# Kernel tuning notes

Hardware: AMD Instinct MI355X
Metric: run time of the kernel (lower is better)

## Reference

```python
import jax, jax.numpy as jnp
import numpy as np

C = 256   # hidden_size (in_channels)
V = 97    # VOC_SIZE + 1
T = 32    # encoder time steps
N = 4096  # batch of text instances


def setup_inputs() -> dict:
    key = jax.random.key(0)
    ks = jax.random.split(key, 10)
    s = lambda k, shape: jax.random.normal(k, shape, dtype=jnp.float32) * 0.05
    return {
        "input": jax.random.randint(ks[0], (N,), 0, V),
        "hidden": s(ks[1], (1, N, C)),
        "encoder_outputs": s(ks[2], (T, N, C)),
        "emb": s(ks[3], (V, C)),
        "combine_w": s(ks[4], (C, 2 * C)), "combine_b": jnp.zeros((C,), jnp.float32),
        "vat_w": s(ks[5], (1, C)), "vat_b": jnp.zeros((1,), jnp.float32),
        "gru_w_ih": s(ks[6], (3 * C, C)), "gru_w_hh": s(ks[7], (3 * C, C)),
        "gru_b_ih": jnp.zeros((3 * C,), jnp.float32), "gru_b_hh": jnp.zeros((3 * C,), jnp.float32),
        "out_w": s(ks[8], (V, C)), "out_b": jnp.zeros((V,), jnp.float32),
    }


def reference(input, hidden, encoder_outputs, emb, combine_w, combine_b,
              vat_w, vat_b, gru_w_ih, gru_w_hh, gru_b_ih, gru_b_hh,
              out_w, out_b):
    # Embedding lookup (dropout = identity in eval mode)
    embedded = emb[input]                                   # [N, C]

    # Bahdanau additive attention: vat(tanh(hidden + enc))
    alpha = jnp.tanh(hidden + encoder_outputs)              # [T, N, C]
    scores = jnp.einsum('tnc,c->nt', alpha, vat_w[0]) + vat_b[0]  # [N, T]
    attn = jax.nn.softmax(scores, axis=1)                   # [N, T]
    applied = jnp.einsum('nt,tnc->nc', attn, encoder_outputs)     # [N, C]

    # Combine + relu
    x = jnp.concatenate([embedded, applied], axis=1) @ combine_w.T + combine_b  # [N, C]
    x = jax.nn.relu(x)

    # Single-step GRU cell (PyTorch gate ordering: r, z, n)
    h = hidden[0]                                           # [N, C]
    gi = x @ gru_w_ih.T + gru_b_ih                          # [N, 3C]
    gh = h @ gru_w_hh.T + gru_b_hh                          # [N, 3C]
    ir, iz, i_n = jnp.split(gi, 3, axis=1)
    hr, hz, h_n = jnp.split(gh, 3, axis=1)
    r = jax.nn.sigmoid(ir + hr)
    z = jax.nn.sigmoid(iz + hz)
    n = jnp.tanh(i_n + r * h_n)
    h_new = (1.0 - z) * n + z * h                           # [N, C]

    out = jax.nn.log_softmax(h_new @ out_w.T + out_b, axis=1)  # [N, V]
    return out, h_new[None, :, :], attn[:, None, :]
```

## Files before the change

kernel.cpp:

```cpp
#include <hip/hip_runtime.h>

typedef unsigned short u16;
using bf16x8 = __attribute__((ext_vector_type(8))) __bf16;
using f32x4  = __attribute__((ext_vector_type(4))) float;

__device__ __forceinline__ u16 f2bf(float f) {
  union { float f; unsigned int i; } v; v.f = f;
  unsigned int r = v.i + 0x7fffu + ((v.i >> 16) & 1u);
  return (u16)(r >> 16);
}
__device__ __forceinline__ void cvt8(u16* dst, const float* src) {
  float4 a0 = *reinterpret_cast<const float4*>(src);
  float4 a1 = *reinterpret_cast<const float4*>(src + 4);
  dst[0] = f2bf(a0.x); dst[1] = f2bf(a0.y); dst[2] = f2bf(a0.z); dst[3] = f2bf(a0.w);
  dst[4] = f2bf(a1.x); dst[5] = f2bf(a1.y); dst[6] = f2bf(a1.z); dst[7] = f2bf(a1.w);
}

__global__ __launch_bounds__(256) void k_attn(
    const float* __restrict__ enc, const float* __restrict__ hid,
    const float* __restrict__ vw, const float* __restrict__ vb,
    const float* __restrict__ emb, const int* __restrict__ inp,
    float* __restrict__ attn_out, u16* __restrict__ Acomb)
{
  __shared__ float enc_s[32 * 260];
  __shared__ float part_s[32 * 8];
  __shared__ float sc_s[32];
  __shared__ float at_s[32];
  __shared__ float h_s[256];
  __shared__ float w_s[256];

  const int n = blockIdx.x;
  const int tid = threadIdx.x;

  #pragma unroll
  for (int it = 0; it < 8; ++it) {
    int ci = tid + it * 256;
    int t = ci >> 6, c4 = ci & 63;
    *reinterpret_cast<float4*>(&enc_s[t * 260 + c4 * 4]) =
      *reinterpret_cast<const float4*>(&enc[(t * 4096 + n) * 256 + c4 * 4]);
  }
  h_s[tid] = hid[n * 256 + tid];
  w_s[tid] = vw[tid];
  __syncthreads();

  {
    int t = tid & 31, p = tid >> 5;
    float s = 0.f;
    for (int j = 0; j < 32; ++j) {
      int c = p * 32 + j;
      s += tanhf(h_s[c] + enc_s[t * 260 + c]) * w_s[c];
    }
    part_s[t * 8 + p] = s;
  }
  __syncthreads();

  if (tid < 32) {
    float sc = vb[0];
    for (int j = 0; j < 8; ++j) sc += part_s[tid * 8 + j];
    sc_s[tid] = sc;
  }
  __syncthreads();

  if (tid < 32) {
    float mx = -1e30f;
    for (int j = 0; j < 32; ++j) mx = fmaxf(mx, sc_s[j]);
    float sum = 0.f;
    for (int j = 0; j < 32; ++j) sum += expf(sc_s[j] - mx);
    float a = expf(sc_s[tid] - mx) / sum;
    at_s[tid] = a;
    attn_out[n * 32 + tid] = a;
  }
  __syncthreads();

  float acc = 0.f;
  for (int t = 0; t < 32; ++t) acc += at_s[t] * enc_s[t * 260 + tid];
  Acomb[n * 512 + 256 + tid] = f2bf(acc);
  Acomb[n * 512 + tid] = f2bf(emb[inp[n] * 256 + tid]);
}

__global__ __launch_bounds__(256) void k_combine(
    const u16* __restrict__ A, const float* __restrict__ W,
    const float* __restrict__ bias, u16* __restrict__ X)
{
  __shared__ u16 As[64 * 40];
  __shared__ u16 Bs[64 * 40];

  const int tid = threadIdx.x;
  const int lane = tid & 63;
  const int wave = tid >> 6;
  const int lr = lane & 15, quad = lane >> 4;
  const int m0 = blockIdx.x * 64;
  const int j0 = blockIdx.y * 64;
  const int wm = (wave & 1) * 32;
  const int wn = (wave >> 1) * 32;
  const int sr = tid >> 2, sq = tid & 3;

  for (int i = tid; i < 64 * 40; i += 256) { As[i] = 0; Bs[i] = 0; }
  __syncthreads();

  f32x4 acc[2][2] = {};

  for (int kt = 0; kt < 16; ++kt) {
    int k0 = kt * 32;
    *reinterpret_cast<uint4*>(&As[sr * 40 + sq * 8]) =
      *reinterpret_cast<const uint4*>(&A[(m0 + sr) * 512 + k0 + sq * 8]);
    cvt8(&Bs[sr * 40 + sq * 8], &W[(j0 + sr) * 512 + k0 + sq * 8]);
    __syncthreads();
    bf16x8 aF[2], bF[2];
    #pragma unroll
    for (int s = 0; s < 2; ++s) {
      aF[s] = *reinterpret_cast<const bf16x8*>(&As[(wm + s * 16 + lr) * 40 + quad * 8]);
      bF[s] = *reinterpret_cast<const bf16x8*>(&Bs[(wn + s * 16 + lr) * 40 + quad * 8]);
    }
    #pragma unroll
    for (int sm = 0; sm < 2; ++sm)
      #pragma unroll
      for (int sn = 0; sn < 2; ++sn)
        acc[sm][sn] = __builtin_amdgcn_mfma_f32_16x16x32_bf16(aF[sm], bF[sn], acc[sm][sn], 0, 0, 0);
    __syncthreads();
  }

  #pragma unroll
  for (int sm = 0; sm < 2; ++sm) {
    #pragma unroll
    for (int sn = 0; sn < 2; ++sn) {
      int gc = j0 + wn + sn * 16 + lr;
      float bv = bias[gc];
      int gr = m0 + wm + sm * 16 + quad * 4;
      #pragma unroll
      for (int r = 0; r < 4; ++r) {
        float v = acc[sm][sn][r] + bv;
        X[(gr + r) * 256 + gc] = f2bf(fmaxf(v, 0.f));
      }
    }
  }
}

__global__ __launch_bounds__(256) void k_gru(
    const u16* __restrict__ X, const float* __restrict__ Hin,
    const float* __restrict__ Wih, const float* __restrict__ Whh,
    const float* __restrict__ bih, const float* __restrict__ bhh,
    float* __restrict__ Hout)
{
  __shared__ u16 Xs[64 * 40];
  __shared__ u16 Hs[64 * 40];
  __shared__ u16 Bs[6 * 32 * 40];

  const int tid = threadIdx.x;
  const int lane = tid & 63;
  const int wave = tid >> 6;
  const int lr = lane & 15, quad = lane >> 4;
  const int m0 = blockIdx.x * 64;
  const int c0 = blockIdx.y * 32;

  for (int i = tid; i < 64 * 40; i += 256) { Xs[i] = 0; Hs[i] = 0; }
  for (int i = tid; i < 6 * 32 * 40; i += 256) Bs[i] = 0;
  __syncthreads();

  f32x4 aI[3][2] = {};
  f32x4 aH[3][2] = {};

  for (int kt = 0; kt < 8; ++kt) {
    int k0 = kt * 32;
    for (int ci = tid; ci < 1280; ci += 256) {
      if (ci < 256) {
        int r = ci >> 2, q = ci & 3;
        *reinterpret_cast<uint4*>(&Xs[r * 40 + q * 8]) =
          *reinterpret_cast<const uint4*>(&X[(m0 + r) * 256 + k0 + q * 8]);
      } else if (ci < 512) {
        int b = ci - 256;
        int r = b >> 2, q = b & 3;
        cvt8(&Hs[r * 40 + q * 8], &Hin[(m0 + r) * 256 + k0 + q * 8]);
      } else {
        int b = ci - 512;
        int g = b >> 7, r = (b >> 2) & 31, q = b & 3;
        const float* Wsrc = (g < 3) ? Wih : Whh;
        int gg = (g < 3) ? g : g - 3;
        cvt8(&Bs[(g * 32 + r) * 40 + q * 8],
             &Wsrc[(gg * 256 + c0 + r) * 256 + k0 + q * 8]);
      }
    }
    __syncthreads();
    bf16x8 xF = *reinterpret_cast<const bf16x8*>(&Xs[(wave * 16 + lr) * 40 + quad * 8]);
    bf16x8 hF = *reinterpret_cast<const bf16x8*>(&Hs[(wave * 16 + lr) * 40 + quad * 8]);
    #pragma unroll
    for (int g = 0; g < 3; ++g) {
      #pragma unroll
      for (int sn = 0; sn < 2; ++sn) {
        bf16x8 bI = *reinterpret_cast<const bf16x8*>(&Bs[(g * 32 + sn * 16 + lr) * 40 + quad * 8]);
        bf16x8 bH = *reinterpret_cast<const bf16x8*>(&Bs[((g + 3) * 32 + sn * 16 + lr) * 40 + quad * 8]);
        aI[g][sn] = __builtin_amdgcn_mfma_f32_16x16x32_bf16(xF, bI, aI[g][sn], 0, 0, 0);
        aH[g][sn] = __builtin_amdgcn_mfma_f32_16x16x32_bf16(hF, bH, aH[g][sn], 0, 0, 0);
      }
    }
    __syncthreads();
  }

  #pragma unroll
  for (int sn = 0; sn < 2; ++sn) {
    int gc = c0 + sn * 16 + lr;
    float b_ir = bih[gc],       b_hr = bhh[gc];
    float b_iz = bih[256 + gc], b_hz = bhh[256 + gc];
    float b_in = bih[512 + gc], b_hn = bhh[512 + gc];
    #pragma unroll
    for (int r = 0; r < 4; ++r) {
      int grow = m0 + wave * 16 + quad * 4 + r;
      float rg = 1.f / (1.f + expf(-(aI[0][sn][r] + b_ir + aH[0][sn][r] + b_hr)));
      float zg = 1.f / (1.f + expf(-(aI[1][sn][r] + b_iz + aH[1][sn][r] + b_hz)));
      float ng = tanhf(aI[2][sn][r] + b_in + rg * (aH[2][sn][r] + b_hn));
      float hv = Hin[grow * 256 + gc];
      Hout[grow * 256 + gc] = (1.f - zg) * ng + zg * hv;
    }
  }
}

__global__ __launch_bounds__(256) void k_out(
    const float* __restrict__ H, const float* __restrict__ Wo,
    const float* __restrict__ bo, float* __restrict__ O)
{
  __shared__ u16 As[64 * 40];
  __shared__ u16 Bs[128 * 40];
  __shared__ float L[64 * 101];
  __shared__ float lz_s[64];

  const int tid = threadIdx.x;
  const int lane = tid & 63;
  const int wave = tid >> 6;
  const int lr = lane & 15, quad = lane >> 4;
  const int m0 = blockIdx.x * 64;

  for (int i = tid; i < 64 * 40; i += 256) As[i] = 0;
  for (int i = tid; i < 128 * 40; i += 256) Bs[i] = 0;
  for (int i = tid; i < 64 * 101; i += 256) L[i] = 0.f;
  if (tid < 64) lz_s[tid] = 0.f;
  __syncthreads();

  f32x4 acc[8] = {};

  for (int kt = 0; kt < 8; ++kt) {
    int k0 = kt * 32;
    {
      int r = tid >> 2, q = tid & 3;
      cvt8(&As[r * 40 + q * 8], &H[(m0 + r) * 256 + k0 + q * 8]);
      #pragma unroll
      for (int it = 0; it < 2; ++it) {
        int ci = tid + it * 256;
        int br = ci >> 2, bq = ci & 3;
        if (br < 97) {
          cvt8(&Bs[br * 40 + bq * 8], &Wo[br * 256 + k0 + bq * 8]);
        } else {
          u16* bd = &Bs[br * 40 + bq * 8];
          #pragma unroll
          for (int z = 0; z < 8; ++z) bd[z] = 0;
        }
      }
    }
    __syncthreads();
    bf16x8 aF = *reinterpret_cast<const bf16x8*>(&As[(wave * 16 + lr) * 40 + quad * 8]);
    #pragma unroll
    for (int s = 0; s < 8; ++s) {
      bf16x8 bF = *reinterpret_cast<const bf16x8*>(&Bs[(s * 16 + lr) * 40 + quad * 8]);
      acc[s] = __builtin_amdgcn_mfma_f32_16x16x32_bf16(aF, bF, acc[s], 0, 0, 0);
    }
    __syncthreads();
  }

  #pragma unroll
  for (int s = 0; s < 8; ++s) {
    int col = s * 16 + lr;
    if (col < 97) {
      float bv = bo[col];
      #pragma unroll
      for (int r = 0; r < 4; ++r) {
        int row = wave * 16 + quad * 4 + r;
        L[row * 101 + col] = acc[s][r] + bv;
      }
    }
  }
  __syncthreads();

  if (tid < 64) {
    float mx = -1e30f;
    for (int c = 0; c < 97; ++c) mx = fmaxf(mx, L[tid * 101 + c]);
    float sum = 0.f;
    for (int c = 0; c < 97; ++c) sum += expf(L[tid * 101 + c] - mx);
    lz_s[tid] = mx + logf(sum);
  }
  __syncthreads();

  {
    int row = tid >> 2, sub = tid & 3;
    float lz = lz_s[row];
    int grow = m0 + row;
    for (int c = sub; c < 97; c += 4)
      O[grow * 97 + c] = L[row * 101 + c] - lz;
  }
}

extern "C" void kernel_launch(void* const* d_in, const int* in_sizes, int n_in,
                              void* d_out, int out_size, void* d_ws, size_t ws_size,
                              hipStream_t stream) {
  const int*   inp = (const int*)d_in[0];
  const float* hid = (const float*)d_in[1];
  const float* enc = (const float*)d_in[2];
  const float* emb = (const float*)d_in[3];
  const float* cw  = (const float*)d_in[4];
  const float* cb  = (const float*)d_in[5];
  const float* vw  = (const float*)d_in[6];
  const float* vb  = (const float*)d_in[7];
  const float* wih = (const float*)d_in[8];
  const float* whh = (const float*)d_in[9];
  const float* bih = (const float*)d_in[10];
  const float* bhh = (const float*)d_in[11];
  const float* ow  = (const float*)d_in[12];
  const float* ob  = (const float*)d_in[13];

  float* out        = (float*)d_out;
  float* out_logits = out;
  float* out_h      = out + 4096 * 97;
  float* out_attn   = out_h + 4096 * 256;

  u16* Acomb = (u16*)d_ws;
  u16* Xbuf  = Acomb + 4096 * 512;

  k_attn<<<4096, 256, 0, stream>>>(enc, hid, vw, vb, emb, inp, out_attn, Acomb);
  k_combine<<<dim3(64, 4), 256, 0, stream>>>(Acomb, cw, cb, Xbuf);
  k_gru<<<dim3(64, 8), 256, 0, stream>>>(Xbuf, hid, wih, whh, bih, bhh, out_h);
  k_out<<<64, 256, 0, stream>>>(out_h, ow, ob, out_logits);
}
```

Measured before the change: 291.1 us.

## Use fast tanh/exp, remap attention scoring, drop smem zeroing, split output kernel

Result: faster. 284.7 us (-2.2%).

```diff
diff --git a/kernel.cpp b/kernel.cpp
--- a/kernel.cpp
+++ b/kernel.cpp
@@ -14,6 +14,13 @@
   float4 a1 = *reinterpret_cast<const float4*>(src + 4);
   dst[0] = f2bf(a0.x); dst[1] = f2bf(a0.y); dst[2] = f2bf(a0.z); dst[3] = f2bf(a0.w);
   dst[4] = f2bf(a1.x); dst[5] = f2bf(a1.y); dst[6] = f2bf(a1.z); dst[7] = f2bf(a1.w);
+}
+__device__ __forceinline__ float ftanh(float x) {
+  float e = __expf(2.f * x);
+  return 1.f - 2.f / (e + 1.f);
+}
+__device__ __forceinline__ float fsigm(float x) {
+  return 1.f / (1.f + __expf(-x));
 }
 
 __global__ __launch_bounds__(256) void k_attn(
@@ -44,11 +51,15 @@
   __syncthreads();
 
   {
-    int t = tid & 31, p = tid >> 5;
+    int t = tid >> 3, p = tid & 7;
+    const float* er = &enc_s[t * 260 + p * 32];
+    const float* hr = &h_s[p * 32];
+    const float* wr = &w_s[p * 32];
     float s = 0.f;
+    #pragma unroll
     for (int j = 0; j < 32; ++j) {
-      int c = p * 32 + j;
-      s += tanhf(h_s[c] + enc_s[t * 260 + c]) * w_s[c];
+      int c = (j + p) & 31;
+      s += ftanh(hr[c] + er[c]) * wr[c];
     }
     part_s[t * 8 + p] = s;
   }
@@ -56,6 +67,7 @@
 
   if (tid < 32) {
     float sc = vb[0];
+    #pragma unroll
     for (int j = 0; j < 8; ++j) sc += part_s[tid * 8 + j];
     sc_s[tid] = sc;
   }
@@ -63,16 +75,19 @@
 
   if (tid < 32) {
     float mx = -1e30f;
+    #pragma unroll
     for (int j = 0; j < 32; ++j) mx = fmaxf(mx, sc_s[j]);
     float sum = 0.f;
-    for (int j = 0; j < 32; ++j) sum += expf(sc_s[j] - mx);
-    float a = expf(sc_s[tid] - mx) / sum;
+    #pragma unroll
+    for (int j = 0; j < 32; ++j) sum += __expf(sc_s[j] - mx);
+    float a = __expf(sc_s[tid] - mx) / sum;
     at_s[tid] = a;
     attn_out[n * 32 + tid] = a;
   }
   __syncthreads();
 
   float acc = 0.f;
+  #pragma unroll
   for (int t = 0; t < 32; ++t) acc += at_s[t] * enc_s[t * 260 + tid];
   Acomb[n * 512 + 256 + tid] = f2bf(acc);
   Acomb[n * 512 + tid] = f2bf(emb[inp[n] * 256 + tid]);
@@ -95,9 +110,6 @@
   const int wn = (wave >> 1) * 32;
   const int sr = tid >> 2, sq = tid & 3;
 
-  for (int i = tid; i < 64 * 40; i += 256) { As[i] = 0; Bs[i] = 0; }
-  __syncthreads();
-
   f32x4 acc[2][2] = {};
 
   for (int kt = 0; kt < 16; ++kt) {
@@ -152,10 +164,6 @@
   const int lr = lane & 15, quad = lane >> 4;
   const int m0 = blockIdx.x * 64;
   const int c0 = blockIdx.y * 32;
-
-  for (int i = tid; i < 64 * 40; i += 256) { Xs[i] = 0; Hs[i] = 0; }
-  for (int i = tid; i < 6 * 32 * 40; i += 256) Bs[i] = 0;
-  __syncthreads();
 
   f32x4 aI[3][2] = {};
   f32x4 aH[3][2] = {};
@@ -205,9 +213,9 @@
     #pragma unroll
     for (int r = 0; r < 4; ++r) {
       int grow = m0 + wave * 16 + quad * 4 + r;
-      float rg = 1.f / (1.f + expf(-(aI[0][sn][r] + b_ir + aH[0][sn][r] + b_hr)));
-      float zg = 1.f / (1.f + expf(-(aI[1][sn][r] + b_iz + aH[1][sn][r] + b_hz)));
-      float ng = tanhf(aI[2][sn][r] + b_in + rg * (aH[2][sn][r] + b_hn));
+      float rg = fsigm(aI[0][sn][r] + b_ir + aH[0][sn][r] + b_hr);
+      float zg = fsigm(aI[1][sn][r] + b_iz + aH[1][sn][r] + b_hz);
+      float ng = ftanh(aI[2][sn][r] + b_in + rg * (aH[2][sn][r] + b_hn));
       float hv = Hin[grow * 256 + gc];
       Hout[grow * 256 + gc] = (1.f - zg) * ng + zg * hv;
     }
@@ -218,82 +226,87 @@
     const float* __restrict__ H, const float* __restrict__ Wo,
     const float* __restrict__ bo, float* __restrict__ O)
 {
-  __shared__ u16 As[64 * 40];
+  __shared__ u16 As[32 * 40];
   __shared__ u16 Bs[128 * 40];
-  __shared__ float L[64 * 101];
-  __shared__ float lz_s[64];
+  __shared__ float L[32 * 101];
+  __shared__ float pm[32 * 8], pl[32 * 8];
+  __shared__ float lz_s[32];
 
   const int tid = threadIdx.x;
   const int lane = tid & 63;
   const int wave = tid >> 6;
   const int lr = lane & 15, quad = lane >> 4;
-  const int m0 = blockIdx.x * 64;
-
-  for (int i = tid; i < 64 * 40; i += 256) As[i] = 0;
-  for (int i = tid; i < 128 * 40; i += 256) Bs[i] = 0;
-  for (int i = tid; i < 64 * 101; i += 256) L[i] = 0.f;
-  if (tid < 64) lz_s[tid] = 0.f;
-  __syncthreads();
-
-  f32x4 acc[8] = {};
+  const int m0 = blockIdx.x * 32;
+  const int rg = (wave >> 1) * 16;
+  const int sg = (wave & 1) * 4;
+
+  for (int i = tid; i < 128 * 40; i += 256) { if ((i / 40) >= 97) Bs[i] = 0; }
+
+  f32x4 acc[4] = {};
 
   for (int kt = 0; kt < 8; ++kt) {
     int k0 = kt * 32;
-    {
+    if (tid < 128) {
       int r = tid >> 2, q = tid & 3;
       cvt8(&As[r * 40 + q * 8], &H[(m0 + r) * 256 + k0 + q * 8]);
-      #pragma unroll
-      for (int it = 0; it < 2; ++it) {
-        int ci = tid + it * 256;
-        int br = ci >> 2, bq = ci & 3;
-        if (br < 97) {
-          cvt8(&Bs[br * 40 + bq * 8], &Wo[br * 256 + k0 + bq * 8]);
-        } else {
-          u16* bd = &Bs[br * 40 + bq * 8];
-          #pragma unroll
-          for (int z = 0; z < 8; ++z) bd[z] = 0;
-        }
-      }
-    }
-    __syncthreads();
-    bf16x8 aF = *reinterpret_cast<const bf16x8*>(&As[(wave * 16 + lr) * 40 + quad * 8]);
-    #pragma unroll
-    for (int s = 0; s < 8; ++s) {
-      bf16x8 bF = *reinterpret_cast<const bf16x8*>(&Bs[(s * 16 + lr) * 40 + quad * 8]);
+    }
+    #pragma unroll
+    for (int it = 0; it < 2; ++it) {
+      int ci = tid + it * 256;
+      int br = ci >> 2, bq = ci & 3;
+      if (br < 97)
+        cvt8(&Bs[br * 40 + bq * 8], &Wo[br * 256 + k0 + bq * 8]);
+    }
+    __syncthreads();
+    bf16x8 aF = *reinterpret_cast<const bf16x8*>(&As[(rg + lr) * 40 + quad * 8]);
+    #pragma unroll
+    for (int s = 0; s < 4; ++s) {
+      bf16x8 bF = *reinterpret_cast<const bf16x8*>(&Bs[((sg + s) * 16 + lr) * 40 + quad * 8]);
       acc[s] = __builtin_amdgcn_mfma_f32_16x16x32_bf16(aF, bF, acc[s], 0, 0, 0);
     }
     __syncthreads();
   }
 
   #pragma unroll
-  for (int s = 0; s < 8; ++s) {
-    int col = s * 16 + lr;
+  for (int s = 0; s < 4; ++s) {
+    int col = (sg + s) * 16 + lr;
     if (col < 97) {
       float bv = bo[col];
       #pragma unroll
-      for (int r = 0; r < 4; ++r) {
-        int row = wave * 16 + quad * 4 + r;
-        L[row * 101 + col] = acc[s][r] + bv;
-      }
-    }
-  }
-  __syncthreads();
-
-  if (tid < 64) {
-    float mx = -1e30f;
-    for (int c = 0; c < 97; ++c) mx = fmaxf(mx, L[tid * 101 + c]);
-    float sum = 0.f;
-    for (int c = 0; c < 97; ++c) sum += expf(L[tid * 101 + c] - mx);
-    lz_s[tid] = mx + logf(sum);
+      for (int r = 0; r < 4; ++r)
+        L[(rg + quad * 4 + r) * 101 + col] = acc[s][r] + bv;
+    }
   }
   __syncthreads();
 
   {
-    int row = tid >> 2, sub = tid & 3;
+    int row = tid >> 3, p = tid & 7;
+    float m = -1e30f, l = 0.f;
+    for (int c = p; c < 97; c += 8) {
+      float v = L[row * 101 + c];
+      if (v > m) { l = l * __expf(m - v) + 1.f; m = v; }
+      else l += __expf(v - m);
+    }
+    pm[row * 8 + p] = m; pl[row * 8 + p] = l;
+  }
+  __syncthreads();
+
+  if (tid < 32) {
+    float M = -1e30f;
+    #pragma unroll
+    for (int p = 0; p < 8; ++p) M = fmaxf(M, pm[tid * 8 + p]);
+    float S = 0.f;
+    #pragma unroll
+    for (int p = 0; p < 8; ++p) S += pl[tid * 8 + p] * __expf(pm[tid * 8 + p] - M);
+    lz_s[tid] = M + __logf(S);
+  }
+  __syncthreads();
+
+  {
+    int row = tid >> 3, p = tid & 7;
     float lz = lz_s[row];
-    int grow = m0 + row;
-    for (int c = sub; c < 97; c += 4)
-      O[grow * 97 + c] = L[row * 101 + c] - lz;
+    for (int c = p; c < 97; c += 8)
+      O[(m0 + row) * 97 + c] = L[row * 101 + c] - lz;
   }
 }
 
@@ -326,5 +339,5 @@
   k_attn<<<4096, 256, 0, stream>>>(enc, hid, vw, vb, emb, inp, out_attn, Acomb);
   k_combine<<<dim3(64, 4), 256, 0, stream>>>(Acomb, cw, cb, Xbuf);
   k_gru<<<dim3(64, 8), 256, 0, stream>>>(Xbuf, hid, wih, whh, bih, bhh, out_h);
-  k_out<<<64, 256, 0, stream>>>(out_h, ow, ob, out_logits);
-}
+  k_out<<<128, 256, 0, stream>>>(out_h, ow, ob, out_logits);
+}
```
